# Kernel tuning notes

Hardware: AMD Instinct MI355X
Metric: run time of the kernel (lower is better)

The kernel has to match this reference:

```python
import jax, jax.numpy as jnp
import numpy as np

D_MODEL = 1024
N_HEADS = 16
D_K = D_MODEL // N_HEADS
B, L = 2, 2048


def setup_inputs() -> dict:
    key = jax.random.key(0)
    ks = jax.random.split(key, 13)
    s = 0.02
    inp = {
        'query': jax.random.normal(ks[0], (B, L, D_MODEL), jnp.float32),
        'key': jax.random.normal(ks[1], (B, L, D_MODEL), jnp.float32),
        'value': jax.random.normal(ks[2], (B, L, D_MODEL), jnp.float32),
        'mask': jax.random.randint(ks[3], (1, 1, L, L), 0, 2).astype(bool),
        'W_q': jax.random.normal(ks[4], (D_MODEL, D_MODEL), jnp.float32) * s,
        'b_q': jnp.zeros((D_MODEL,), jnp.float32),
        'W_k': jax.random.normal(ks[5], (D_MODEL, D_MODEL), jnp.float32) * s,
        'b_k': jnp.zeros((D_MODEL,), jnp.float32),
        'W_v': jax.random.normal(ks[6], (D_MODEL, D_MODEL), jnp.float32) * s,
        'b_v': jnp.zeros((D_MODEL,), jnp.float32),
        'W_o': jax.random.normal(ks[7], (D_MODEL, D_MODEL), jnp.float32) * s,
        'b_o': jnp.zeros((D_MODEL,), jnp.float32),
    }
    return inp


def _split_heads(x):
    b, l, _ = x.shape
    return x.reshape(b, l, N_HEADS, D_K).transpose(0, 2, 1, 3)  # [B,H,L,dk]


def reference(query, key, value, mask, W_q, b_q, W_k, b_k, W_v, b_v, W_o, b_o):
    q = _split_heads(query @ W_q + b_q)
    k = _split_heads(key @ W_k + b_k)
    v = _split_heads(value @ W_v + b_v)
    # Unscaled attention logits [B,H,L,L] (NO 1/sqrt(dk))
    logits = jnp.einsum('bhqd,bhkd->bhqk', q, k)
    logits = jnp.where(mask, -jnp.inf, logits)
    w = jax.nn.softmax(logits, axis=-1)
    w = jnp.nan_to_num(w, nan=0.0)  # fully-masked rows -> zeros
    attended = jnp.einsum('bhqk,bhkd->bhqd', w, v)
    # dropout in eval mode = identity; combine heads
    out = attended.transpose(0, 2, 1, 3).reshape(B, L, D_MODEL)
    return out @ W_o + b_o
```

## Files before the change

kernel.cpp:

```cpp
#include <hip/hip_runtime.h>
#include <hip/hip_bf16.h>
#include <stdint.h>


typedef __bf16 bf16;
typedef __bf16 bf16x8 __attribute__((ext_vector_type(8)));
typedef float f32x4 __attribute__((ext_vector_type(4)));

#define AS1 __attribute__((address_space(1)))
#define AS3 __attribute__((address_space(3)))

__device__ __forceinline__ void g2l16(const void* g, void* l) {
    __builtin_amdgcn_global_load_lds((AS1 void*)g, (AS3 void*)l, 16, 0, 0);
}

#define LOG2E 1.44269504088896f

__global__ __launch_bounds__(256) void cvt3_kernel(const float* __restrict__ a0,
                                                   const float* __restrict__ a1,
                                                   const float* __restrict__ a2,
                                                   bf16* o0, bf16* o1, bf16* o2) {
    int y = blockIdx.y;
    const float* in = (y == 0) ? a0 : (y == 1) ? a1 : a2;
    bf16* out = (y == 0) ? o0 : (y == 1) ? o1 : o2;
    int idx = blockIdx.x * 256 + threadIdx.x;
    float4 v = ((const float4*)in)[idx];
    __align__(8) bf16 o[4];
    o[0] = (bf16)v.x; o[1] = (bf16)v.y; o[2] = (bf16)v.z; o[3] = (bf16)v.w;
    *(uint2*)(out + (size_t)idx * 4) = *(const uint2*)o;
}

__global__ __launch_bounds__(256) void mdetect_kernel(const unsigned int* __restrict__ w,
                                                      int* __restrict__ flag) {
    int idx = blockIdx.x * 256 + threadIdx.x;
    unsigned v = w[idx];
    int f = 0;
    if (v == 0x3F800000u) f = 2;
    else if (v > 1u) f = 1;
    unsigned long long b1 = __ballot(f & 1);
    unsigned long long b2 = __ballot(f & 2);
    if ((threadIdx.x & 63) == 0) {
        int agg = (b1 ? 1 : 0) | (b2 ? 2 : 0);
        if (agg) atomicOr(flag, agg);
    }
}

__global__ __launch_bounds__(256) void mpack_kernel(const void* __restrict__ mask,
                                                    unsigned long long* __restrict__ mb,
                                                    const int* __restrict__ flag) {
    int idx = blockIdx.x * 256 + threadIdx.x;
    int f = *flag;
    bool v;
    if (f & 2)      v = ((const float*)mask)[idx] != 0.0f;
    else if (f & 1) v = ((const unsigned char*)mask)[idx] != 0;
    else            v = ((const int*)mask)[idx] != 0;
    unsigned long long b = __ballot(v);
    if ((threadIdx.x & 63) == 0) mb[idx >> 6] = b;
}

__global__ __launch_bounds__(256) void wtrans_kernel(const float* W0, const float* W1,
                                                     const float* W2, const float* W3,
                                                     bf16* T0, bf16* T1, bf16* T2, bf16* T3) {
    const float* W; bf16* T;
    int y = blockIdx.y;
    if (y == 0)      { W = W0; T = T0; }
    else if (y == 1) { W = W1; T = T1; }
    else if (y == 2) { W = W2; T = T2; }
    else             { W = W3; T = T3; }
    int tx = blockIdx.x & 15, ty = blockIdx.x >> 4;
    int n0 = tx * 64, k0 = ty * 64;
    __shared__ __align__(16) bf16 t[64 * 72];
    int tid = threadIdx.x;
    #pragma unroll
    for (int rr = 0; rr < 4; ++rr) {
        int idx = rr * 256 + tid;
        int r = idx >> 4, c4 = (idx & 15) * 4;
        float4 v = *(const float4*)(W + (size_t)(k0 + r) * 1024 + n0 + c4);
        __align__(8) bf16 o[4];
        o[0] = (bf16)v.x; o[1] = (bf16)v.y; o[2] = (bf16)v.z; o[3] = (bf16)v.w;
        *(uint2*)&t[r * 72 + c4] = *(const uint2*)o;
    }
    __syncthreads();
    #pragma unroll
    for (int rr = 0; rr < 2; ++rr) {
        int idx = rr * 256 + tid;
        int n = idx >> 3, kc = (idx & 7) * 8;
        __align__(16) bf16 o[8];
        #pragma unroll
        for (int j = 0; j < 8; ++j) o[j] = t[(kc + j) * 72 + n];
        *(uint4*)(T + (size_t)(n0 + n) * 1024 + k0 + kc) = *(const uint4*)o;
    }
}

template <int MODE>
__device__ __forceinline__ void gemm128_core(const bf16* __restrict__ A,
                                             const bf16* __restrict__ Bt,
                                             const float* __restrict__ bias,
                                             void* __restrict__ Out, int bm, int bn,
                                             float scale) {
    __shared__ __align__(16) bf16 la[128 * 32];
    __shared__ __align__(16) bf16 lb[128 * 32];
    int tid = threadIdx.x;
    int w = tid >> 6, lane = tid & 63;
    int quad = lane >> 4, col = lane & 15;
    int wm = w >> 1, wn = w & 1;
    int m0 = bm * 128, n0 = bn * 128;
    f32x4 acc[4][4];
    f32x4 z = {0.f, 0.f, 0.f, 0.f};
    #pragma unroll
    for (int i = 0; i < 4; ++i)
        #pragma unroll
        for (int j = 0; j < 4; ++j) acc[i][j] = z;
    int srow = lane >> 2;
    int skc = (lane & 3) * 8;
    for (int kt = 0; kt < 32; ++kt) {
        int kk = kt * 32;
        __syncthreads();
        #pragma unroll
        for (int rr = 0; rr < 2; ++rr) {
            int ch = rr * 4 + w;
            int row = ch * 16 + srow;
            g2l16(A + (size_t)(m0 + row) * 1024 + kk + skc, &la[ch * 512]);
            g2l16(Bt + (size_t)(n0 + row) * 1024 + kk + skc, &lb[ch * 512]);
        }
        __syncthreads();
        bf16x8 af[4], bfr[4];
        #pragma unroll
        for (int mt = 0; mt < 4; ++mt)
            af[mt] = *(const bf16x8*)&la[(wm * 64 + mt * 16 + col) * 32 + quad * 8];
        #pragma unroll
        for (int nt = 0; nt < 4; ++nt)
            bfr[nt] = *(const bf16x8*)&lb[(wn * 64 + nt * 16 + col) * 32 + quad * 8];
        #pragma unroll
        for (int mt = 0; mt < 4; ++mt)
            #pragma unroll
            for (int nt = 0; nt < 4; ++nt)
                acc[mt][nt] = __builtin_amdgcn_mfma_f32_16x16x32_bf16(
                    af[mt], bfr[nt], acc[mt][nt], 0, 0, 0);
    }
    float bia[4];
    #pragma unroll
    for (int nt = 0; nt < 4; ++nt) bia[nt] = bias[n0 + wn * 64 + nt * 16 + col];
    #pragma unroll
    for (int mt = 0; mt < 4; ++mt) {
        #pragma unroll
        for (int nt = 0; nt < 4; ++nt) {
            #pragma unroll
            for (int r = 0; r < 4; ++r) {
                int m = m0 + wm * 64 + mt * 16 + quad * 4 + r;
                int n = n0 + wn * 64 + nt * 16 + col;
                float v = (acc[mt][nt][r] + bia[nt]) * scale;
                if (MODE == 0) {
                    int b = m >> 11, l = m & 2047, h = n >> 6, d = n & 63;
                    ((bf16*)Out)[(((size_t)b * 16 + h) * 2048 + l) * 64 + d] = (bf16)v;
                } else {
                    int b = m >> 11, l = m & 2047, h = n >> 6, d = n & 63;
                    ((bf16*)Out)[(((size_t)b * 16 + h) * 64 + d) * 2048 + l] = (bf16)v;
                }
            }
        }
    }
}

__global__ __launch_bounds__(256) void qkv_kernel(
    const bf16* Xq, const bf16* Xk, const bf16* Xv,
    const bf16* Wq, const bf16* Wk, const bf16* Wv,
    const float* bq, const float* bk, const float* bv,
    bf16* Qh, bf16* Kh, bf16* Vt) {
    int y = blockIdx.y;
    int bm = blockIdx.x >> 3, bn = blockIdx.x & 7;
    if (y == 0)      gemm128_core<0>(Xq, Wq, bq, Qh, bm, bn, LOG2E);
    else if (y == 1) gemm128_core<0>(Xk, Wk, bk, Kh, bm, bn, 1.0f);
    else             gemm128_core<2>(Xv, Wv, bv, Vt, bm, bn, 1.0f);
}

__global__ __launch_bounds__(256) void ogemm_kernel(const bf16* __restrict__ A,
                                                    const bf16* __restrict__ Wt,
                                                    const float* __restrict__ bias,
                                                    float* __restrict__ Out) {
    int bm = blockIdx.x >> 3, bn = blockIdx.x & 7;
    __shared__ __align__(16) bf16 la[64 * 32];
    __shared__ __align__(16) bf16 lb[128 * 32];
    int tid = threadIdx.x;
    int w = tid >> 6, lane = tid & 63;
    int quad = lane >> 4, col = lane & 15;
    int m0 = bm * 64, n0 = bn * 128;
    f32x4 acc[4][2];
    f32x4 z = {0.f, 0.f, 0.f, 0.f};
    #pragma unroll
    for (int i = 0; i < 4; ++i) { acc[i][0] = z; acc[i][1] = z; }
    int srow = lane >> 2;
    int skc = (lane & 3) * 8;
    for (int kt = 0; kt < 32; ++kt) {
        int kk = kt * 32;
        __syncthreads();
        g2l16(A + (size_t)(m0 + w * 16 + srow) * 1024 + kk + skc, &la[w * 512]);
        #pragma unroll
        for (int rr = 0; rr < 2; ++rr) {
            int ch = rr * 4 + w;
            g2l16(Wt + (size_t)(n0 + ch * 16 + srow) * 1024 + kk + skc, &lb[ch * 512]);
        }
        __syncthreads();
        bf16x8 af[4], bfr[2];
        #pragma unroll
        for (int mt = 0; mt < 4; ++mt)
            af[mt] = *(const bf16x8*)&la[(mt * 16 + col) * 32 + quad * 8];
        #pragma unroll
        for (int nt = 0; nt < 2; ++nt)
            bfr[nt] = *(const bf16x8*)&lb[(w * 32 + nt * 16 + col) * 32 + quad * 8];
        #pragma unroll
        for (int mt = 0; mt < 4; ++mt)
            #pragma unroll
            for (int nt = 0; nt < 2; ++nt)
                acc[mt][nt] = __builtin_amdgcn_mfma_f32_16x16x32_bf16(
                    af[mt], bfr[nt], acc[mt][nt], 0, 0, 0);
    }
    float bia[2];
    bia[0] = bias[n0 + w * 32 + col];
    bia[1] = bias[n0 + w * 32 + 16 + col];
    #pragma unroll
    for (int mt = 0; mt < 4; ++mt)
        #pragma unroll
        for (int nt = 0; nt < 2; ++nt)
            #pragma unroll
            for (int r = 0; r < 4; ++r)
                Out[(size_t)(m0 + mt * 16 + quad * 4 + r) * 1024 +
                    n0 + w * 32 + nt * 16 + col] = acc[mt][nt][r] + bia[nt];
}

__global__ __launch_bounds__(256) void attn_kernel(const bf16* __restrict__ Qh,
                                                   const bf16* __restrict__ Kh,
                                                   const bf16* __restrict__ Vt,
                                                   const unsigned long long* __restrict__ mb,
                                                   bf16* __restrict__ att) {
    int bh = blockIdx.x, qt = blockIdx.y;
    int b = bh >> 4, h = bh & 15;
    int q0 = qt * 128;
    __shared__ __align__(16) bf16 qs[128 * 64];
    __shared__ __align__(16) bf16 ks[64 * 64];
    __shared__ __align__(16) bf16 vs[64 * 64];
    __shared__ __align__(16) bf16 ps[4 * 32 * 72];
    int tid = threadIdx.x;
    int w = tid >> 6, lane = tid & 63;
    int quad = lane >> 4, col = lane & 15;
    int c7 = col & 7;
    int sr = lane >> 3;
    int sg = (lane & 7) ^ sr;
    int swz0 = (quad ^ c7) * 8;
    int swz1 = ((4 + quad) ^ c7) * 8;

    #pragma unroll
    for (int i = 0; i < 4; ++i) {
        int ch = w * 4 + i;
        g2l16(Qh + ((size_t)bh * 2048 + q0 + ch * 8 + sr) * 64 + sg * 8, &qs[ch * 512]);
    }
    __syncthreads();
    bf16x8 aq[2][2];
    #pragma unroll
    for (int mt = 0; mt < 2; ++mt) {
        aq[mt][0] = *(const bf16x8*)&qs[(w * 32 + mt * 16 + col) * 64 + swz0];
        aq[mt][1] = *(const bf16x8*)&qs[(w * 32 + mt * 16 + col) * 64 + swz1];
    }

    f32x4 z = {0.f, 0.f, 0.f, 0.f};
    f32x4 O[2][4];
    float rs[2][4];
    #pragma unroll
    for (int mt = 0; mt < 2; ++mt)
        #pragma unroll
        for (int i = 0; i < 4; ++i) { O[mt][i] = z; rs[mt][i] = 0.f; }

    for (int kt = 0; kt < 32; ++kt) {
        __syncthreads();
        #pragma unroll
        for (int rr = 0; rr < 2; ++rr) {
            int ch = rr * 4 + w;
            int r = ch * 8 + sr;
            g2l16(Kh + ((size_t)bh * 2048 + kt * 64 + r) * 64 + sg * 8, &ks[ch * 512]);
            g2l16(Vt + ((size_t)bh * 64 + r) * 2048 + kt * 64 + sg * 8, &vs[ch * 512]);
        }
        __syncthreads();

        f32x4 s[2][4];
        #pragma unroll
        for (int nt = 0; nt < 4; ++nt) {
            s[0][nt] = z; s[1][nt] = z;
            bf16x8 bk0 = *(const bf16x8*)&ks[(nt * 16 + col) * 64 + swz0];
            s[0][nt] = __builtin_amdgcn_mfma_f32_16x16x32_bf16(aq[0][0], bk0, s[0][nt], 0, 0, 0);
            s[1][nt] = __builtin_amdgcn_mfma_f32_16x16x32_bf16(aq[1][0], bk0, s[1][nt], 0, 0, 0);
            bf16x8 bk1 = *(const bf16x8*)&ks[(nt * 16 + col) * 64 + swz1];
            s[0][nt] = __builtin_amdgcn_mfma_f32_16x16x32_bf16(aq[0][1], bk1, s[0][nt], 0, 0, 0);
            s[1][nt] = __builtin_amdgcn_mfma_f32_16x16x32_bf16(aq[1][1], bk1, s[1][nt], 0, 0, 0);
        }

        #pragma unroll
        for (int mt = 0; mt < 2; ++mt) {
            #pragma unroll
            for (int r = 0; r < 4; ++r) {
                unsigned long long t =
                    mb[(size_t)(q0 + w * 32 + mt * 16 + quad * 4 + r) * 32 + kt] >> col;
                #pragma unroll
                for (int nt = 0; nt < 4; ++nt) {
                    float p = __builtin_amdgcn_exp2f(s[mt][nt][r]);
                    if ((t >> (nt * 16)) & 1ull) p = 0.0f;
                    rs[mt][r] += p;
                    ps[w * 2304 + (mt * 16 + quad * 4 + r) * 72 + nt * 16 + col] = (bf16)p;
                }
            }
        }

        bf16x8 ap[2][2];
        #pragma unroll
        for (int mt = 0; mt < 2; ++mt) {
            ap[mt][0] = *(const bf16x8*)&ps[w * 2304 + (mt * 16 + col) * 72 + quad * 8];
            ap[mt][1] = *(const bf16x8*)&ps[w * 2304 + (mt * 16 + col) * 72 + 32 + quad * 8];
        }
        #pragma unroll
        for (int dt = 0; dt < 4; ++dt) {
            bf16x8 bv0 = *(const bf16x8*)&vs[(dt * 16 + col) * 64 + swz0];
            O[0][dt] = __builtin_amdgcn_mfma_f32_16x16x32_bf16(ap[0][0], bv0, O[0][dt], 0, 0, 0);
            O[1][dt] = __builtin_amdgcn_mfma_f32_16x16x32_bf16(ap[1][0], bv0, O[1][dt], 0, 0, 0);
            bf16x8 bv1 = *(const bf16x8*)&vs[(dt * 16 + col) * 64 + swz1];
            O[0][dt] = __builtin_amdgcn_mfma_f32_16x16x32_bf16(ap[0][1], bv1, O[0][dt], 0, 0, 0);
            O[1][dt] = __builtin_amdgcn_mfma_f32_16x16x32_bf16(ap[1][1], bv1, O[1][dt], 0, 0, 0);
        }
    }

    #pragma unroll
    for (int mt = 0; mt < 2; ++mt)
        #pragma unroll
        for (int r = 0; r < 4; ++r)
            #pragma unroll
            for (int d = 1; d < 16; d <<= 1) rs[mt][r] += __shfl_xor(rs[mt][r], d);

    #pragma unroll
    for (int mt = 0; mt < 2; ++mt) {
        #pragma unroll
        for (int r = 0; r < 4; ++r) {
            float inv = (rs[mt][r] > 0.f) ? 1.0f / rs[mt][r] : 0.f;
            int qg = q0 + w * 32 + mt * 16 + quad * 4 + r;
            #pragma unroll
            for (int dt = 0; dt < 4; ++dt) {
                float ov = O[mt][dt][r] * inv;
                att[((size_t)b * 2048 + qg) * 1024 + h * 64 + dt * 16 + col] = (bf16)ov;
            }
        }
    }
}

extern "C" void kernel_launch(void* const* d_in, const int* in_sizes, int n_in,
                              void* d_out, int out_size, void* d_ws, size_t ws_size,
                              hipStream_t stream) {
    (void)in_sizes; (void)n_in; (void)out_size; (void)ws_size;
    const float* query = (const float*)d_in[0];
    const float* key_  = (const float*)d_in[1];
    const float* value = (const float*)d_in[2];
    const void*  mask  = d_in[3];
    const float* W_q = (const float*)d_in[4];
    const float* b_q = (const float*)d_in[5];
    const float* W_k = (const float*)d_in[6];
    const float* b_k = (const float*)d_in[7];
    const float* W_v = (const float*)d_in[8];
    const float* b_v = (const float*)d_in[9];
    const float* W_o = (const float*)d_in[10];
    const float* b_o = (const float*)d_in[11];

    char* ws = (char*)d_ws;
    bf16* Xq  = (bf16*)(ws + 0);
    bf16* Xk  = (bf16*)(ws + 8388608);
    bf16* Xv  = (bf16*)(ws + 16777216);
    bf16* Wtq = (bf16*)(ws + 25165824);
    bf16* Wtk = (bf16*)(ws + 27262976);
    bf16* Wtv = (bf16*)(ws + 29360128);
    bf16* Wto = (bf16*)(ws + 31457280);
    bf16* Qh  = (bf16*)(ws + 33554432);
    bf16* Kh  = (bf16*)(ws + 41943040);
    bf16* Vt  = (bf16*)(ws + 50331648);
    bf16* att = (bf16*)(ws + 58720256);
    unsigned long long* mb = (unsigned long long*)(ws + 67108864);
    int* flag = (int*)(ws + 67633152);

    hipMemsetAsync(flag, 0, 4, stream);
    mdetect_kernel<<<4096, 256, 0, stream>>>((const unsigned int*)mask, flag);
    mpack_kernel<<<16384, 256, 0, stream>>>(mask, mb, flag);

    cvt3_kernel<<<dim3(4096, 3), 256, 0, stream>>>(query, key_, value, Xq, Xk, Xv);
    wtrans_kernel<<<dim3(256, 4), 256, 0, stream>>>(W_q, W_k, W_v, W_o, Wtq, Wtk, Wtv, Wto);

    qkv_kernel<<<dim3(256, 3), 256, 0, stream>>>(Xq, Xk, Xv, Wtq, Wtk, Wtv,
                                                 b_q, b_k, b_v, Qh, Kh, Vt);
    attn_kernel<<<dim3(32, 16), 256, 0, stream>>>(Qh, Kh, Vt, mb, att);
    ogemm_kernel<<<512, 256, 0, stream>>>(att, Wto, b_o, (float*)d_out);
}
```

Baseline: 274.4 us.

## Repack mask into per-MFMA-fragment ballots and compute row sums via MFMA

Adds a pre-pass that repacks the bit mask so that each 16x16 MFMA output fragment has one wave-uniform 64-bit word, letting the attention kernel test masking with a scalar load plus inverse ballot. The old path did per-lane 64-bit loads and shifts. Row sums of the probabilities now come from an extra MFMA against a ones vector instead of per-element adds and a cross-lane shuffle reduction. The cost is an extra small kernel launch, 4 extra MFMAs per tile, and sums taken over bf16-rounded probabilities.

```diff
diff --git a/kernel.cpp b/kernel.cpp
--- a/kernel.cpp
+++ b/kernel.cpp
@@ -12,6 +12,14 @@
 
 __device__ __forceinline__ void g2l16(const void* g, void* l) {
     __builtin_amdgcn_global_load_lds((AS1 void*)g, (AS3 void*)l, 16, 0, 0);
+}
+
+__device__ __forceinline__ bool lane_masked(unsigned long long m) {
+#if __has_builtin(__builtin_amdgcn_inverse_ballot_w64)
+    return __builtin_amdgcn_inverse_ballot_w64(m);
+#else
+    return (m >> (threadIdx.x & 63)) & 1ull;
+#endif
 }
 
 #define LOG2E 1.44269504088896f
@@ -56,6 +64,22 @@
     else            v = ((const int*)mask)[idx] != 0;
     unsigned long long b = __ballot(v);
     if ((threadIdx.x & 63) == 0) mb[idx >> 6] = b;
+}
+
+__global__ __launch_bounds__(256) void rpack_kernel(const unsigned long long* __restrict__ mb,
+                                                    unsigned long long* __restrict__ rmb) {
+    int task = blockIdx.x * 4 + (threadIdx.x >> 6);
+    int qg = task >> 5, kt = task & 31;
+    int lane = threadIdx.x & 63, quad = lane >> 4, col = lane & 15;
+    #pragma unroll
+    for (int r = 0; r < 4; ++r) {
+        unsigned long long wrow = mb[(size_t)(qg * 16 + quad * 4 + r) * 32 + kt];
+        #pragma unroll
+        for (int nt = 0; nt < 4; ++nt) {
+            unsigned long long b = __ballot(((wrow >> (nt * 16 + col)) & 1ull) != 0);
+            if (lane == 0) rmb[(size_t)task * 16 + r * 4 + nt] = b;
+        }
+    }
 }
 
 __global__ __launch_bounds__(256) void wtrans_kernel(const float* W0, const float* W1,
@@ -231,7 +255,7 @@
 __global__ __launch_bounds__(256) void attn_kernel(const bf16* __restrict__ Qh,
                                                    const bf16* __restrict__ Kh,
                                                    const bf16* __restrict__ Vt,
-                                                   const unsigned long long* __restrict__ mb,
+                                                   const unsigned long long* __restrict__ rmb,
                                                    bf16* __restrict__ att) {
     int bh = blockIdx.x, qt = blockIdx.y;
     int b = bh >> 4, h = bh & 15;
@@ -249,6 +273,8 @@
     int swz0 = (quad ^ c7) * 8;
     int swz1 = ((4 + quad) ^ c7) * 8;
 
+    int mofs = __builtin_amdgcn_readfirstlane((qt * 8 + w * 2) * 512);
+
     #pragma unroll
     for (int i = 0; i < 4; ++i) {
         int ch = w * 4 + i;
@@ -261,14 +287,18 @@
         aq[mt][0] = *(const bf16x8*)&qs[(w * 32 + mt * 16 + col) * 64 + swz0];
         aq[mt][1] = *(const bf16x8*)&qs[(w * 32 + mt * 16 + col) * 64 + swz1];
     }
+    bf16x8 onesf;
+    #pragma unroll
+    for (int i = 0; i < 8; ++i) onesf[i] = (bf16)1.0f;
 
     f32x4 z = {0.f, 0.f, 0.f, 0.f};
-    f32x4 O[2][4];
-    float rs[2][4];
-    #pragma unroll
-    for (int mt = 0; mt < 2; ++mt)
-        #pragma unroll
-        for (int i = 0; i < 4; ++i) { O[mt][i] = z; rs[mt][i] = 0.f; }
+    f32x4 O[2][4], R[2];
+    #pragma unroll
+    for (int mt = 0; mt < 2; ++mt) {
+        R[mt] = z;
+        #pragma unroll
+        for (int i = 0; i < 4; ++i) O[mt][i] = z;
+    }
 
     for (int kt = 0; kt < 32; ++kt) {
         __syncthreads();
@@ -295,15 +325,13 @@
 
         #pragma unroll
         for (int mt = 0; mt < 2; ++mt) {
+            const unsigned long long* mw = rmb + mofs + mt * 512 + kt * 16;
             #pragma unroll
             for (int r = 0; r < 4; ++r) {
-                unsigned long long t =
-                    mb[(size_t)(q0 + w * 32 + mt * 16 + quad * 4 + r) * 32 + kt] >> col;
                 #pragma unroll
                 for (int nt = 0; nt < 4; ++nt) {
                     float p = __builtin_amdgcn_exp2f(s[mt][nt][r]);
-                    if ((t >> (nt * 16)) & 1ull) p = 0.0f;
-                    rs[mt][r] += p;
+                    if (lane_masked(mw[r * 4 + nt])) p = 0.0f;
                     ps[w * 2304 + (mt * 16 + quad * 4 + r) * 72 + nt * 16 + col] = (bf16)p;
                 }
             }
@@ -324,20 +352,19 @@
             O[0][dt] = __builtin_amdgcn_mfma_f32_16x16x32_bf16(ap[0][1], bv1, O[0][dt], 0, 0, 0);
             O[1][dt] = __builtin_amdgcn_mfma_f32_16x16x32_bf16(ap[1][1], bv1, O[1][dt], 0, 0, 0);
         }
-    }
-
-    #pragma unroll
-    for (int mt = 0; mt < 2; ++mt)
-        #pragma unroll
-        for (int r = 0; r < 4; ++r)
-            #pragma unroll
-            for (int d = 1; d < 16; d <<= 1) rs[mt][r] += __shfl_xor(rs[mt][r], d);
+        #pragma unroll
+        for (int mt = 0; mt < 2; ++mt) {
+            R[mt] = __builtin_amdgcn_mfma_f32_16x16x32_bf16(ap[mt][0], onesf, R[mt], 0, 0, 0);
+            R[mt] = __builtin_amdgcn_mfma_f32_16x16x32_bf16(ap[mt][1], onesf, R[mt], 0, 0, 0);
+        }
+    }
 
     #pragma unroll
     for (int mt = 0; mt < 2; ++mt) {
         #pragma unroll
         for (int r = 0; r < 4; ++r) {
-            float inv = (rs[mt][r] > 0.f) ? 1.0f / rs[mt][r] : 0.f;
+            float rsv = R[mt][r];
+            float inv = (rsv > 0.f) ? 1.0f / rsv : 0.f;
             int qg = q0 + w * 32 + mt * 16 + quad * 4 + r;
             #pragma unroll
             for (int dt = 0; dt < 4; ++dt) {
@@ -377,18 +404,20 @@
     bf16* Kh  = (bf16*)(ws + 41943040);
     bf16* Vt  = (bf16*)(ws + 50331648);
     bf16* att = (bf16*)(ws + 58720256);
-    unsigned long long* mb = (unsigned long long*)(ws + 67108864);
-    int* flag = (int*)(ws + 67633152);
+    unsigned long long* mb  = (unsigned long long*)(ws + 67108864);
+    unsigned long long* rmb = (unsigned long long*)(ws + 67633152);
+    int* flag = (int*)(ws + 68157440);
 
     hipMemsetAsync(flag, 0, 4, stream);
     mdetect_kernel<<<4096, 256, 0, stream>>>((const unsigned int*)mask, flag);
     mpack_kernel<<<16384, 256, 0, stream>>>(mask, mb, flag);
+    rpack_kernel<<<1024, 256, 0, stream>>>(mb, rmb);
 
     cvt3_kernel<<<dim3(4096, 3), 256, 0, stream>>>(query, key_, value, Xq, Xk, Xv);
     wtrans_kernel<<<dim3(256, 4), 256, 0, stream>>>(W_q, W_k, W_v, W_o, Wtq, Wtk, Wtv, Wto);
 
     qkv_kernel<<<dim3(256, 3), 256, 0, stream>>>(Xq, Xk, Xv, Wtq, Wtk, Wtv,
                                                  b_q, b_k, b_v, Qh, Kh, Vt);
-    attn_kernel<<<dim3(32, 16), 256, 0, stream>>>(Qh, Kh, Vt, mb, att);
+    attn_kernel<<<dim3(32, 16), 256, 0, stream>>>(Qh, Kh, Vt, rmb, att);
     ogemm_kernel<<<512, 256, 0, stream>>>(att, Wto, b_o, (float*)d_out);
 }
```

New measurement: 295.3 us. +7.6%, slower.
